# Kernel tuning notes

Hardware: AMD Instinct MI355X
Metric: run time of the kernel (lower is better)

## Reference

```python
import jax, jax.numpy as jnp
import numpy as np

L, H, LATENT, DM, DH, FF = 4, 4, 256, 768, 192, 1024
EPS = 1e-6      # fast_transformers RecurrentLinearAttention eps
LN_EPS = 1e-5


def make_pe(d_model=LATENT, max_len=5000):
    pos = np.arange(max_len, dtype=np.float32)[:, None]
    div = np.exp(np.arange(0, d_model, 2, dtype=np.float32) * (-np.log(10000.0) / d_model))
    pe = np.zeros((max_len, d_model), np.float32)
    pe[:, 0::2] = np.sin(pos * div)
    pe[:, 1::2] = np.cos(pos * div)
    return jnp.asarray(pe)

PE = make_pe()


def layer_norm(x, g, b):
    m = x.mean(-1, keepdims=True)
    v = ((x - m) ** 2).mean(-1, keepdims=True)
    return (x - m) * jax.lax.rsqrt(v + LN_EPS) * g + b


def setup_inputs() -> dict:
    key = jax.random.key(0)
    ks = jax.random.split(key, 16)
    bs, nj, nf, T, A, C = 8, 25, 6, 80, 6, 12
    s = 0.02
    return dict(
        x=jax.random.normal(ks[0], (bs, nj, nf, T), jnp.float32),
        y=jax.random.randint(ks[1], (bs, A), 0, C),
        ind_map=jnp.sort(jax.random.randint(ks[2], (T, bs), 0, A), axis=0),
        act_tstamps=jnp.sort(jax.random.randint(ks[3], (bs, A), 1, T + 1), axis=1).at[:, -1].set(T),
        skel_W=jax.random.normal(ks[4], (nj * nf, LATENT), jnp.float32) * s,
        skel_b=jnp.zeros((LATENT,), jnp.float32),
        muQuery=jax.random.normal(ks[5], (C, LATENT), jnp.float32),
        sigmaQuery=jax.random.normal(ks[6], (C, LATENT), jnp.float32),
        Wq=jax.random.normal(ks[7], (L, DM, DM), jnp.float32) * s,
        bq=jnp.zeros((L, DM), jnp.float32),
        Wk=jax.random.normal(ks[8], (L, DM, DM), jnp.float32) * s,
        bk=jnp.zeros((L, DM), jnp.float32),
        Wv=jax.random.normal(ks[9], (L, DM, DM), jnp.float32) * s,
        bv=jnp.zeros((L, DM), jnp.float32),
        Wo=jax.random.normal(ks[10], (L, DM, DM), jnp.float32) * s,
        bo=jnp.zeros((L, DM), jnp.float32),
        W1=jax.random.normal(ks[11], (L, DM, FF), jnp.float32) * s,
        b1=jnp.zeros((L, FF), jnp.float32),
        W2=jax.random.normal(ks[12], (L, FF, DM), jnp.float32) * s,
        b2=jnp.zeros((L, DM), jnp.float32),
        ln1_g=jnp.ones((L, DM), jnp.float32), ln1_b=jnp.zeros((L, DM), jnp.float32),
        ln2_g=jnp.ones((L, DM), jnp.float32), ln2_b=jnp.zeros((L, DM), jnp.float32),
        lnf_g=jnp.ones((DM,), jnp.float32), lnf_b=jnp.zeros((DM,), jnp.float32),
    )


def _fwd(x, y, ind_map, act_tstamps, skel_W, skel_b, muQuery, sigmaQuery,
         Wq, bq, Wk, bk, Wv, bv, Wo, bo, W1, b1, W2, b2,
         ln1_g, ln1_b, ln2_g, ln2_b, lnf_g, lnf_b):
    bs, nj, nf, T = x.shape
    # skeleton embedding: [T, bs, njoints*nfeats] @ W -> [T, bs, LATENT]
    xe = x.transpose(3, 0, 1, 2).reshape(T, bs, nj * nf) @ skel_W + skel_b
    mu_q = muQuery[y]        # [bs, A, LATENT]
    sig_q = sigmaQuery[y]
    barange = jnp.arange(bs)

    @jax.checkpoint
    def step(carry, inputs):
        S, Z = carry                         # [L,bs,H,DH,DH], [L,bs,H,DH]
        t, xt, ind_t = inputs
        cm = mu_q[barange, ind_t]            # gather per-sample current action query
        cs = sig_q[barange, ind_t]
        xseq = jnp.stack([cm, cs, xt], 0)    # [3, bs, LATENT]
        start = jnp.where(t == 0, 0, t + 2)  # PositionalEncoding(last_pos=t, offset=2)
        pe3 = jax.lax.dynamic_slice_in_dim(PE, start, 3, 0)
        xseq = xseq + pe3[:, None, :]
        h = xseq.transpose(1, 0, 2).reshape(bs, 3 * LATENT)  # flatten -> [bs, DM]
        nS, nZ = [], []
        for l in range(L):
            q = (h @ Wq[l] + bq[l]).reshape(bs, H, DH)
            k = (h @ Wk[l] + bk[l]).reshape(bs, H, DH)
            v = (h @ Wv[l] + bv[l]).reshape(bs, H, DH)
            Q = jax.nn.elu(q) + 1.0          # linear-attention feature map
            K = jax.nn.elu(k) + 1.0
            Sl = S[l] + K[..., :, None] * v[..., None, :]   # state update S += k (x) v
            Zl = Z[l] + K
            inv = 1.0 / (jnp.einsum('bhd,bhd->bh', Q, Zl) + EPS)
            att = jnp.einsum('bhd,bhdm,bh->bhm', Q, Sl, inv).reshape(bs, DM)
            h1 = layer_norm(h + att @ Wo[l] + bo[l], ln1_g[l], ln1_b[l])
            ffn = jax.nn.relu(h1 @ W1[l] + b1[l]) @ W2[l] + b2[l]
            h = layer_norm(h1 + ffn, ln2_g[l], ln2_b[l])
            nS.append(Sl); nZ.append(Zl)
        h = layer_norm(h, lnf_g, lnf_b)      # encoder final norm
        return (jnp.stack(nS), jnp.stack(nZ)), h

    S0 = jnp.zeros((L, bs, H, DH, DH), x.dtype)
    Z0 = jnp.zeros((L, bs, H, DH), x.dtype)
    _, finals = jax.lax.scan(step, (S0, Z0), (jnp.arange(T), xe, ind_map))  # finals: [T,bs,DM]
    tsel = jnp.maximum(act_tstamps - 1, 0)                       # [bs, A]
    mu = finals[:, :, :LATENT][tsel, barange[:, None]]           # [bs, A, LATENT]
    logvar = finals[:, :, LATENT:2 * LATENT][tsel, barange[:, None]]
    return mu, logvar


def reference(x, y, ind_map, act_tstamps, skel_W, skel_b, muQuery, sigmaQuery,
              Wq, bq, Wk, bk, Wv, bv, Wo, bo, W1, b1, W2, b2,
              ln1_g, ln1_b, ln2_g, ln2_b, lnf_g, lnf_b):
    return _fwd(x, y, ind_map, act_tstamps, skel_W, skel_b, muQuery, sigmaQuery,
                Wq, bq, Wk, bk, Wv, bv, Wo, bo, W1, b1, W2, b2,
                ln1_g, ln1_b, ln2_g, ln2_b, lnf_g, lnf_b)
```

## Files before the change

### kernel.cpp

```cpp
#include <hip/hip_runtime.h>
#include <math.h>

#define TT 80
#define BS 8
#define NA 6
#define DMODEL 768
#define NH 4
#define DH 192
#define FFD 1024
#define NROWS (TT*BS)
#define NQKV (3*DMODEL)

typedef __bf16 bf16;
typedef __bf16 bf16x8 __attribute__((ext_vector_type(8)));
typedef float  f32x4  __attribute__((ext_vector_type(4)));

__device__ __forceinline__ float block_reduce_sum256(float v, float* sm4) {
#pragma unroll
    for (int off = 32; off > 0; off >>= 1) v += __shfl_down(v, off, 64);
    int lane = threadIdx.x & 63, wid = threadIdx.x >> 6;
    if (lane == 0) sm4[wid] = v;
    __syncthreads();
    float r = sm4[0] + sm4[1] + sm4[2] + sm4[3];
    __syncthreads();
    return r;
}

__global__ __launch_bounds__(256) void embed_k(
        const float* __restrict__ x, const int* __restrict__ y,
        const int* __restrict__ ind_map, const float* __restrict__ skel_W,
        const float* __restrict__ skel_b, const float* __restrict__ muQ,
        const float* __restrict__ sigQ, float* __restrict__ h0,
        bf16* __restrict__ h0b) {
    __shared__ float xrow[152];
    int r = blockIdx.x;
    int t = r >> 3, b = r & 7;
    int c = threadIdx.x;
    if (c < 150) xrow[c] = x[(b * 150 + c) * TT + t];
    __syncthreads();
    float acc = skel_b[c];
    for (int jf = 0; jf < 150; jf++) acc += xrow[jf] * skel_W[jf * 256 + c];
    int ind_t = ind_map[t * 8 + b];
    int yb = y[b * NA + ind_t];
    float cm = muQ[yb * 256 + c];
    float cs = sigQ[yb * 256 + c];
    int start = (t == 0) ? 0 : (t + 2);
    float div = expf((float)(c & ~1) * (-9.210340371976184f / 256.0f));
    float p0, p1, p2;
    if (c & 1) {
        p0 = cosf((float)start * div);
        p1 = cosf((float)(start + 1) * div);
        p2 = cosf((float)(start + 2) * div);
    } else {
        p0 = sinf((float)start * div);
        p1 = sinf((float)(start + 1) * div);
        p2 = sinf((float)(start + 2) * div);
    }
    float* hr = h0 + (size_t)r * DMODEL;
    float v0 = cm + p0, v1 = cs + p1, v2 = acc + p2;
    hr[c] = v0; hr[c + 256] = v1; hr[c + 512] = v2;
    bf16* hb = h0b + (size_t)r * DMODEL;
    hb[c] = (bf16)v0; hb[c + 256] = (bf16)v1; hb[c + 512] = (bf16)v2;
}

__global__ __launch_bounds__(256) void transpose_k(
        const float* __restrict__ Wq, const float* __restrict__ Wk,
        const float* __restrict__ Wv, const float* __restrict__ Wo,
        const float* __restrict__ W1, const float* __restrict__ W2,
        bf16* __restrict__ qkvT, bf16* __restrict__ woT,
        bf16* __restrict__ w1T, bf16* __restrict__ w2T) {
    int lz = blockIdx.z;
    int l = lz >> 2, z = lz & 3;
    int K = (z == 3) ? 1024 : 768;
    int N = (z == 0) ? 2304 : (z == 2) ? 1024 : 768;
    int k0 = blockIdx.x * 32, n0 = blockIdx.y * 32;
    if (k0 >= K || n0 >= N) return;
    const float* src; bf16* dst; int ldsrc; int ncol;
    if (z == 0) {
        if (n0 < 768)       { src = Wq + (size_t)l * 768 * 768; ncol = n0; }
        else if (n0 < 1536) { src = Wk + (size_t)l * 768 * 768; ncol = n0 - 768; }
        else                { src = Wv + (size_t)l * 768 * 768; ncol = n0 - 1536; }
        dst = qkvT + (size_t)l * NQKV * DMODEL; ldsrc = 768;
    } else if (z == 1) { src = Wo + (size_t)l * 768 * 768;  dst = woT + (size_t)l * 768 * 768;  ldsrc = 768;  ncol = n0; }
    else if (z == 2)   { src = W1 + (size_t)l * 768 * 1024; dst = w1T + (size_t)l * 1024 * 768; ldsrc = 1024; ncol = n0; }
    else               { src = W2 + (size_t)l * 1024 * 768; dst = w2T + (size_t)l * 768 * 1024; ldsrc = 768;  ncol = n0; }
    __shared__ float tile[32][33];
    int tx = threadIdx.x & 31, ty = threadIdx.x >> 5;
#pragma unroll
    for (int i = 0; i < 4; i++) {
        int r = ty + 8 * i;
        tile[r][tx] = src[(size_t)(k0 + r) * ldsrc + ncol + tx];
    }
    __syncthreads();
#pragma unroll
    for (int i = 0; i < 4; i++) {
        int r = ty + 8 * i;
        dst[(size_t)(n0 + r) * K + k0 + tx] = (bf16)tile[tx][r];
    }
}

template <int EPI>
__global__ __launch_bounds__(256) void gemm_mfma(
        const bf16* __restrict__ A, const bf16* __restrict__ Bt,
        const float* __restrict__ bias_q, const float* __restrict__ bias_k,
        const float* __restrict__ bias_v, const float* __restrict__ resid,
        float* __restrict__ outF, bf16* __restrict__ outB,
        int M, int N, int K) {
    __shared__ __attribute__((aligned(16))) bf16 As0[64][40];
    __shared__ __attribute__((aligned(16))) bf16 As1[64][40];
    __shared__ __attribute__((aligned(16))) bf16 Bs0[64][40];
    __shared__ __attribute__((aligned(16))) bf16 Bs1[64][40];
    int tid = threadIdx.x;
    int m0 = blockIdx.y * 64, n0 = blockIdx.x * 64;
    int w = tid >> 6;
    int l = tid & 63;
    int lm = l & 15, lq = l >> 4;
    int sr = tid >> 2;
    int sk = (tid & 3) * 8;
    const bf16* Arow = &A[(size_t)(m0 + sr) * K];
    const bf16* Brow = &Bt[(size_t)(n0 + sr) * K];
    f32x4 acc[4] = {};
    uint4 a0 = *(const uint4*)&Arow[sk];
    uint4 a1 = *(const uint4*)&Arow[32 + sk];
    uint4 b0 = *(const uint4*)&Brow[sk];
    uint4 b1 = *(const uint4*)&Brow[32 + sk];
    for (int k0 = 0; k0 < K; k0 += 64) {
        __syncthreads();
        *(uint4*)&As0[sr][sk] = a0;
        *(uint4*)&As1[sr][sk] = a1;
        *(uint4*)&Bs0[sr][sk] = b0;
        *(uint4*)&Bs1[sr][sk] = b1;
        __syncthreads();
        int k2 = k0 + 64; if (k2 >= K) k2 = 0;
        a0 = *(const uint4*)&Arow[k2 + sk];
        a1 = *(const uint4*)&Arow[k2 + 32 + sk];
        b0 = *(const uint4*)&Brow[k2 + sk];
        b1 = *(const uint4*)&Brow[k2 + 32 + sk];
        bf16x8 af0 = *(bf16x8*)&As0[w * 16 + lm][lq * 8];
        bf16x8 af1 = *(bf16x8*)&As1[w * 16 + lm][lq * 8];
#pragma unroll
        for (int nb = 0; nb < 4; nb++) {
            bf16x8 bf0 = *(bf16x8*)&Bs0[nb * 16 + lm][lq * 8];
            acc[nb] = __builtin_amdgcn_mfma_f32_16x16x32_bf16(af0, bf0, acc[nb], 0, 0, 0);
        }
#pragma unroll
        for (int nb = 0; nb < 4; nb++) {
            bf16x8 bf1 = *(bf16x8*)&Bs1[nb * 16 + lm][lq * 8];
            acc[nb] = __builtin_amdgcn_mfma_f32_16x16x32_bf16(af1, bf1, acc[nb], 0, 0, 0);
        }
    }
#pragma unroll
    for (int nb = 0; nb < 4; nb++) {
        int col = n0 + nb * 16 + lm;
        float b;
        bool do_elu = false;
        if (EPI == 0) {
            if (col < 768)       { b = bias_q[col];        do_elu = true; }
            else if (col < 1536) { b = bias_k[col - 768];  do_elu = true; }
            else                 { b = bias_v[col - 1536]; }
        } else {
            b = bias_q[col];
        }
#pragma unroll
        for (int r = 0; r < 4; r++) {
            int row = m0 + w * 16 + lq * 4 + r;
            float v = acc[nb][r] + b;
            if (EPI == 0) {
                if (do_elu) v = (v > 0.0f) ? (v + 1.0f) : expf(v);
                outB[(size_t)row * N + col] = (bf16)v;
            } else if (EPI == 1) {
                v += resid[(size_t)row * N + col];
                outF[(size_t)row * N + col] = v;
            } else {
                v = fmaxf(v, 0.0f);
                outB[(size_t)row * N + col] = (bf16)v;
            }
        }
    }
}

__global__ __launch_bounds__(256) void ln_k(
        const float* __restrict__ in, float* __restrict__ outF,
        bf16* __restrict__ outB,
        const float* __restrict__ g, const float* __restrict__ b) {
    int wave = threadIdx.x >> 6, lane = threadIdx.x & 63;
    int row = blockIdx.x * 4 + wave;
    const float* xr = in + (size_t)row * DMODEL;
    float4 v[3];
    float s = 0.0f;
#pragma unroll
    for (int j = 0; j < 3; j++) {
        v[j] = *(const float4*)&xr[lane * 4 + 256 * j];
        s += v[j].x + v[j].y + v[j].z + v[j].w;
    }
#pragma unroll
    for (int mk = 1; mk < 64; mk <<= 1) s += __shfl_xor(s, mk, 64);
    float m = s * (1.0f / 768.0f);
    float sq = 0.0f;
#pragma unroll
    for (int j = 0; j < 3; j++) {
        v[j].x -= m; v[j].y -= m; v[j].z -= m; v[j].w -= m;
        sq += v[j].x * v[j].x + v[j].y * v[j].y + v[j].z * v[j].z + v[j].w * v[j].w;
    }
#pragma unroll
    for (int mk = 1; mk < 64; mk <<= 1) sq += __shfl_xor(sq, mk, 64);
    float r = rsqrtf(sq * (1.0f / 768.0f) + 1e-5f);
    float* orow = outF + (size_t)row * DMODEL;
    bf16* brow = outB + (size_t)row * DMODEL;
#pragma unroll
    for (int j = 0; j < 3; j++) {
        int c = lane * 4 + 256 * j;
        float4 gg = *(const float4*)&g[c];
        float4 bb = *(const float4*)&b[c];
        float o0 = v[j].x * r * gg.x + bb.x;
        float o1 = v[j].y * r * gg.y + bb.y;
        float o2 = v[j].z * r * gg.z + bb.z;
        float o3 = v[j].w * r * gg.w + bb.w;
        *(float4*)&orow[c] = make_float4(o0, o1, o2, o3);
        bf16 tmp4[4] = {(bf16)o0, (bf16)o1, (bf16)o2, (bf16)o3};
        *(uint2*)&brow[c] = *(uint2*)tmp4;
    }
}

__global__ __launch_bounds__(320) void attn_k(
        const bf16* __restrict__ qkvB, bf16* __restrict__ att) {
    __shared__ __attribute__((aligned(16))) char smem[64000];
    bf16* Qs = (bf16*)smem;
    bf16* Ks = (bf16*)(smem + 32000);
    bf16* Aij = (bf16*)smem;
    bf16* VT = (bf16*)(smem + 16640);

    int b = blockIdx.x >> 2, h = blockIdx.x & 3;
    int tid = threadIdx.x;
    int w = tid >> 6, l = tid & 63;
    int lm = l & 15, lq = l >> 4;

    uint4 vreg[6];
#pragma unroll
    for (int u = 0; u < 6; u++) {
        int c = tid + 320 * u;
        int t = c / 24, cc = c % 24;
        int d0 = cc * 8;
        size_t g = (size_t)(t * 8 + b) * NQKV + h * DH + d0;
        uint4 qv = *(const uint4*)&qkvB[g];
        uint4 kv = *(const uint4*)&qkvB[g + 768];
        vreg[u]  = *(const uint4*)&qkvB[g + 1536];
        *(uint4*)&Qs[t * 200 + d0] = qv;
        *(uint4*)&Ks[t * 200 + d0] = kv;
    }
    __syncthreads();

    f32x4 acc[5] = {};
#pragma unroll
    for (int k0 = 0; k0 < 192; k0 += 32) {
        bf16x8 af = *(bf16x8*)&Qs[(w * 16 + lm) * 200 + lq * 8 + k0];
#pragma unroll
        for (int nb = 0; nb < 5; nb++) {
            bf16x8 bfr = *(bf16x8*)&Ks[(nb * 16 + lm) * 200 + lq * 8 + k0];
            acc[nb] = __builtin_amdgcn_mfma_f32_16x16x32_bf16(af, bfr, acc[nb], 0, 0, 0);
        }
    }
    float mval[5][4];
    float rs[4] = {0.f, 0.f, 0.f, 0.f};
#pragma unroll
    for (int nb = 0; nb < 5; nb++)
#pragma unroll
        for (int r = 0; r < 4; r++) {
            int t = w * 16 + lq * 4 + r, tau = nb * 16 + lm;
            float v = (tau <= t) ? acc[nb][r] : 0.0f;
            mval[nb][r] = v;
            rs[r] += v;
        }
#pragma unroll
    for (int mk = 1; mk < 16; mk <<= 1)
#pragma unroll
        for (int r = 0; r < 4; r++) rs[r] += __shfl_xor(rs[r], mk, 64);
    float inv[4];
#pragma unroll
    for (int r = 0; r < 4; r++) inv[r] = 1.0f / (rs[r] + 1e-6f);

    __syncthreads();

#pragma unroll
    for (int nb = 0; nb < 5; nb++)
#pragma unroll
        for (int r = 0; r < 4; r++)
            Aij[(w * 16 + lq * 4 + r) * 104 + nb * 16 + lm] = (bf16)mval[nb][r];
    *(uint2*)&Aij[(tid >> 2) * 104 + 80 + (tid & 3) * 4] = make_uint2(0u, 0u);
#pragma unroll
    for (int u = 0; u < 6; u++) {
        int c = tid + 320 * u;
        int t = c / 24, cc = c % 24;
        int d0 = cc * 8;
        bf16 tmp8[8];
        *(uint4*)tmp8 = vreg[u];
#pragma unroll
        for (int j = 0; j < 8; j++) VT[(d0 + j) * 104 + t] = tmp8[j];
    }
    if (tid < 192) {
        *(uint4*)&VT[tid * 104 + 80] = make_uint4(0u, 0u, 0u, 0u);
        *(uint4*)&VT[tid * 104 + 88] = make_uint4(0u, 0u, 0u, 0u);
    }
    __syncthreads();

#pragma unroll 1
    for (int nc = 0; nc < 12; nc++) {
        f32x4 a2 = {};
#pragma unroll
        for (int k0 = 0; k0 < 96; k0 += 32) {
            bf16x8 af = *(bf16x8*)&Aij[(w * 16 + lm) * 104 + lq * 8 + k0];
            bf16x8 bfr = *(bf16x8*)&VT[(nc * 16 + lm) * 104 + lq * 8 + k0];
            a2 = __builtin_amdgcn_mfma_f32_16x16x32_bf16(af, bfr, a2, 0, 0, 0);
        }
#pragma unroll
        for (int r = 0; r < 4; r++) {
            int t = w * 16 + lq * 4 + r;
            att[(size_t)(t * 8 + b) * DMODEL + h * DH + nc * 16 + lm] =
                (bf16)(a2[r] * inv[r]);
        }
    }
}

__global__ __launch_bounds__(256) void final_k(
        const float* __restrict__ h, const int* __restrict__ act_ts,
        const float* __restrict__ g, const float* __restrict__ bb,
        float* __restrict__ out) {
    __shared__ float sm4[4];
    int ba = blockIdx.x;
    int b = ba / NA;
    int ts = act_ts[ba];
    int t = ts - 1; if (t < 0) t = 0;
    const float* xr = h + (size_t)(t * 8 + b) * DMODEL;
    int c = threadIdx.x;
    float x0 = xr[c], x1 = xr[c + 256], x2 = xr[c + 512];
    float m = block_reduce_sum256(x0 + x1 + x2, sm4) * (1.0f / 768.0f);
    float d0 = x0 - m, d1 = x1 - m, d2 = x2 - m;
    float v = block_reduce_sum256(d0 * d0 + d1 * d1 + d2 * d2, sm4) * (1.0f / 768.0f);
    float r = rsqrtf(v + 1e-5f);
    out[ba * 256 + c]            = d0 * r * g[c] + bb[c];
    out[48 * 256 + ba * 256 + c] = d1 * r * g[c + 256] + bb[c + 256];
}

extern "C" void kernel_launch(void* const* d_in, const int* in_sizes, int n_in,
                              void* d_out, int out_size, void* d_ws, size_t ws_size,
                              hipStream_t stream) {
    const float* x       = (const float*)d_in[0];
    const int*   y       = (const int*)d_in[1];
    const int*   ind_map = (const int*)d_in[2];
    const int*   act_ts  = (const int*)d_in[3];
    const float* skel_W  = (const float*)d_in[4];
    const float* skel_b  = (const float*)d_in[5];
    const float* muQ     = (const float*)d_in[6];
    const float* sigQ    = (const float*)d_in[7];
    const float* Wq = (const float*)d_in[8];   const float* bq = (const float*)d_in[9];
    const float* Wk = (const float*)d_in[10];  const float* bk = (const float*)d_in[11];
    const float* Wv = (const float*)d_in[12];  const float* bv = (const float*)d_in[13];
    const float* Wo = (const float*)d_in[14];  const float* bo = (const float*)d_in[15];
    const float* W1 = (const float*)d_in[16];  const float* b1 = (const float*)d_in[17];
    const float* W2 = (const float*)d_in[18];  const float* b2 = (const float*)d_in[19];
    const float* ln1_g = (const float*)d_in[20]; const float* ln1_b = (const float*)d_in[21];
    const float* ln2_g = (const float*)d_in[22]; const float* ln2_b = (const float*)d_in[23];
    const float* lnf_g = (const float*)d_in[24]; const float* lnf_b = (const float*)d_in[25];
    float* out = (float*)d_out;

    char* p = (char*)d_ws;
    const size_t R  = (size_t)NROWS * DMODEL;
    float* h    = (float*)p; p += R * 4;
    float* h1   = (float*)p; p += R * 4;
    float* tmp  = (float*)p; p += R * 4;
    bf16* qkvB  = (bf16*)p;  p += (size_t)NROWS * NQKV * 2;
    bf16* hB    = (bf16*)p;  p += R * 2;
    bf16* h1B   = (bf16*)p;  p += R * 2;
    bf16* attB  = (bf16*)p;  p += R * 2;
    bf16* ffn1B = (bf16*)p;  p += (size_t)NROWS * FFD * 2;
    bf16* qkvT  = (bf16*)p;  p += (size_t)4 * NQKV * DMODEL * 2;
    bf16* woT   = (bf16*)p;  p += (size_t)4 * DMODEL * DMODEL * 2;
    bf16* w1T   = (bf16*)p;  p += (size_t)4 * FFD * DMODEL * 2;
    bf16* w2T   = (bf16*)p;  p += (size_t)4 * DMODEL * FFD * 2;

    dim3 gT(32, 72, 16);
    transpose_k<<<gT, 256, 0, stream>>>(Wq, Wk, Wv, Wo, W1, W2, qkvT, woT, w1T, w2T);
    embed_k<<<NROWS, 256, 0, stream>>>(x, y, ind_map, skel_W, skel_b, muQ, sigQ, h, hB);

    dim3 gQKV(NQKV / 64, 10);
    dim3 g768(12, 10);
    dim3 g1024(16, 10);
    for (int l = 0; l < 4; l++) {
        const bf16* qkvTl = qkvT + (size_t)l * NQKV * DMODEL;
        const bf16* woTl  = woT  + (size_t)l * DMODEL * DMODEL;
        const bf16* w1Tl  = w1T  + (size_t)l * FFD * DMODEL;
        const bf16* w2Tl  = w2T  + (size_t)l * DMODEL * FFD;
        gemm_mfma<0><<<gQKV, 256, 0, stream>>>(hB, qkvTl,
                bq + l * DMODEL, bk + l * DMODEL, bv + l * DMODEL,
                nullptr, nullptr, qkvB, NROWS, NQKV, DMODEL);
        attn_k<<<32, 320, 0, stream>>>(qkvB, attB);
        gemm_mfma<1><<<g768, 256, 0, stream>>>(attB, woTl,
                bo + l * DMODEL, nullptr, nullptr, h, tmp, nullptr,
                NROWS, DMODEL, DMODEL);
        ln_k<<<NROWS / 4, 256, 0, stream>>>(tmp, h1, h1B, ln1_g + l * DMODEL, ln1_b + l * DMODEL);
        gemm_mfma<2><<<g1024, 256, 0, stream>>>(h1B, w1Tl,
                b1 + l * FFD, nullptr, nullptr, nullptr, nullptr, ffn1B,
                NROWS, FFD, DMODEL);
        gemm_mfma<1><<<g768, 256, 0, stream>>>(ffn1B, w2Tl,
                b2 + l * DMODEL, nullptr, nullptr, h1, tmp, nullptr,
                NROWS, DMODEL, FFD);
        ln_k<<<NROWS / 4, 256, 0, stream>>>(tmp, h, hB, ln2_g + l * DMODEL, ln2_b + l * DMODEL);
    }

    final_k<<<48, 256, 0, stream>>>(h, act_ts, lnf_g, lnf_b, out);
}
```

Baseline: 422.5 us.

## Fuse LayerNorm into GEMM epilogue stats and next GEMM's A-load prologue

Removes the standalone LayerNorm kernels. The residual GEMMs now accumulate per-row sum and sum-of-squares through atomics in their epilogue. The following GEMM then normalizes its fp32 A operand on the fly while staging it into shared memory, and one column-block writes out the normalized fp32 rows for later residual use. This saves two launches per layer and one full read/write pass of the activations. In exchange the A loads are fp32, twice the bytes, every column block repeats the normalization, the stats need a memset, and the one-pass E[x^2]-mean^2 variance is less numerically robust.

Result: slower. 464.6 us (+10.0%).

```diff
diff --git a/kernel.cpp b/kernel.cpp
--- a/kernel.cpp
+++ b/kernel.cpp
@@ -99,12 +99,16 @@
     }
 }
 
-template <int EPI>
+template <int AMODE, int EPI>
 __global__ __launch_bounds__(256) void gemm_mfma(
-        const bf16* __restrict__ A, const bf16* __restrict__ Bt,
-        const float* __restrict__ bias_q, const float* __restrict__ bias_k,
-        const float* __restrict__ bias_v, const float* __restrict__ resid,
+        const void* __restrict__ Asrc, const bf16* __restrict__ Bt,
+        const float* __restrict__ bias0, const float* __restrict__ bias1,
+        const float* __restrict__ bias2, const float* __restrict__ resid,
+        const float* __restrict__ inS, const float* __restrict__ inQ,
+        const float* __restrict__ ag, const float* __restrict__ ab,
+        float* __restrict__ aNormOut,
         float* __restrict__ outF, bf16* __restrict__ outB,
+        float* __restrict__ outS, float* __restrict__ outQ,
         int M, int N, int K) {
     __shared__ __attribute__((aligned(16))) bf16 As0[64][40];
     __shared__ __attribute__((aligned(16))) bf16 As1[64][40];
@@ -117,23 +121,77 @@
     int lm = l & 15, lq = l >> 4;
     int sr = tid >> 2;
     int sk = (tid & 3) * 8;
-    const bf16* Arow = &A[(size_t)(m0 + sr) * K];
+    const bf16* Ab = nullptr; const float* Af = nullptr;
+    float mn = 0.0f, rs = 0.0f;
+    if (AMODE == 0) {
+        Ab = (const bf16*)Asrc + (size_t)(m0 + sr) * K;
+    } else {
+        Af = (const float*)Asrc + (size_t)(m0 + sr) * 768;
+        float s = inS[m0 + sr], q = inQ[m0 + sr];
+        mn = s * (1.0f / 768.0f);
+        rs = rsqrtf(q * (1.0f / 768.0f) - mn * mn + 1e-5f);
+    }
     const bf16* Brow = &Bt[(size_t)(n0 + sr) * K];
+    bool awrite = (AMODE == 1) && (blockIdx.x == 0);
     f32x4 acc[4] = {};
-    uint4 a0 = *(const uint4*)&Arow[sk];
-    uint4 a1 = *(const uint4*)&Arow[32 + sk];
-    uint4 b0 = *(const uint4*)&Brow[sk];
-    uint4 b1 = *(const uint4*)&Brow[32 + sk];
+    uint4 a0, a1, a2, a3, b0, b1;
+    if (AMODE == 0) {
+        a0 = *(const uint4*)&Ab[sk];
+        a1 = *(const uint4*)&Ab[32 + sk];
+    } else {
+        a0 = *(const uint4*)&Af[sk];      a1 = *(const uint4*)&Af[sk + 4];
+        a2 = *(const uint4*)&Af[32 + sk]; a3 = *(const uint4*)&Af[32 + sk + 4];
+    }
+    b0 = *(const uint4*)&Brow[sk];
+    b1 = *(const uint4*)&Brow[32 + sk];
     for (int k0 = 0; k0 < K; k0 += 64) {
         __syncthreads();
-        *(uint4*)&As0[sr][sk] = a0;
-        *(uint4*)&As1[sr][sk] = a1;
+        if (AMODE == 0) {
+            *(uint4*)&As0[sr][sk] = a0;
+            *(uint4*)&As1[sr][sk] = a1;
+        } else {
+#pragma unroll
+            for (int half = 0; half < 2; half++) {
+                int kabs = k0 + 32 * half;
+                float4 v0 = *(float4*)(half ? &a2 : &a0);
+                float4 v1 = *(float4*)(half ? &a3 : &a1);
+                float4 gg0 = *(const float4*)&ag[kabs + sk];
+                float4 gg1 = *(const float4*)&ag[kabs + sk + 4];
+                float4 bb0 = *(const float4*)&ab[kabs + sk];
+                float4 bb1 = *(const float4*)&ab[kabs + sk + 4];
+                float o[8];
+                o[0] = (v0.x - mn) * rs * gg0.x + bb0.x;
+                o[1] = (v0.y - mn) * rs * gg0.y + bb0.y;
+                o[2] = (v0.z - mn) * rs * gg0.z + bb0.z;
+                o[3] = (v0.w - mn) * rs * gg0.w + bb0.w;
+                o[4] = (v1.x - mn) * rs * gg1.x + bb1.x;
+                o[5] = (v1.y - mn) * rs * gg1.y + bb1.y;
+                o[6] = (v1.z - mn) * rs * gg1.z + bb1.z;
+                o[7] = (v1.w - mn) * rs * gg1.w + bb1.w;
+                if (awrite) {
+                    *(float4*)&aNormOut[(size_t)(m0 + sr) * 768 + kabs + sk] =
+                        make_float4(o[0], o[1], o[2], o[3]);
+                    *(float4*)&aNormOut[(size_t)(m0 + sr) * 768 + kabs + sk + 4] =
+                        make_float4(o[4], o[5], o[6], o[7]);
+                }
+                bf16 t8[8];
+#pragma unroll
+                for (int j = 0; j < 8; j++) t8[j] = (bf16)o[j];
+                if (half) *(uint4*)&As1[sr][sk] = *(uint4*)t8;
+                else      *(uint4*)&As0[sr][sk] = *(uint4*)t8;
+            }
+        }
         *(uint4*)&Bs0[sr][sk] = b0;
         *(uint4*)&Bs1[sr][sk] = b1;
         __syncthreads();
         int k2 = k0 + 64; if (k2 >= K) k2 = 0;
-        a0 = *(const uint4*)&Arow[k2 + sk];
-        a1 = *(const uint4*)&Arow[k2 + 32 + sk];
+        if (AMODE == 0) {
+            a0 = *(const uint4*)&Ab[k2 + sk];
+            a1 = *(const uint4*)&Ab[k2 + 32 + sk];
+        } else {
+            a0 = *(const uint4*)&Af[k2 + sk];      a1 = *(const uint4*)&Af[k2 + sk + 4];
+            a2 = *(const uint4*)&Af[k2 + 32 + sk]; a3 = *(const uint4*)&Af[k2 + 32 + sk + 4];
+        }
         b0 = *(const uint4*)&Brow[k2 + sk];
         b1 = *(const uint4*)&Brow[k2 + 32 + sk];
         bf16x8 af0 = *(bf16x8*)&As0[w * 16 + lm][lq * 8];
@@ -149,76 +207,60 @@
             acc[nb] = __builtin_amdgcn_mfma_f32_16x16x32_bf16(af1, bf1, acc[nb], 0, 0, 0);
         }
     }
-#pragma unroll
-    for (int nb = 0; nb < 4; nb++) {
-        int col = n0 + nb * 16 + lm;
-        float b;
-        bool do_elu = false;
-        if (EPI == 0) {
-            if (col < 768)       { b = bias_q[col];        do_elu = true; }
-            else if (col < 1536) { b = bias_k[col - 768];  do_elu = true; }
-            else                 { b = bias_v[col - 1536]; }
-        } else {
-            b = bias_q[col];
-        }
-#pragma unroll
-        for (int r = 0; r < 4; r++) {
-            int row = m0 + w * 16 + lq * 4 + r;
-            float v = acc[nb][r] + b;
+    if (EPI == 3) {
+        float s[4] = {0.f, 0.f, 0.f, 0.f}, q[4] = {0.f, 0.f, 0.f, 0.f};
+#pragma unroll
+        for (int nb = 0; nb < 4; nb++) {
+            int col = n0 + nb * 16 + lm;
+            float bia = bias0[col];
+#pragma unroll
+            for (int r = 0; r < 4; r++) {
+                int row = m0 + w * 16 + lq * 4 + r;
+                float v = acc[nb][r] + bia + resid[(size_t)row * N + col];
+                outF[(size_t)row * N + col] = v;
+                s[r] += v; q[r] += v * v;
+            }
+        }
+#pragma unroll
+        for (int mk = 1; mk < 16; mk <<= 1)
+#pragma unroll
+            for (int r = 0; r < 4; r++) {
+                s[r] += __shfl_xor(s[r], mk, 64);
+                q[r] += __shfl_xor(q[r], mk, 64);
+            }
+        if (lm == 0) {
+#pragma unroll
+            for (int r = 0; r < 4; r++) {
+                int row = m0 + w * 16 + lq * 4 + r;
+                atomicAdd(&outS[row], s[r]);
+                atomicAdd(&outQ[row], q[r]);
+            }
+        }
+    } else {
+#pragma unroll
+        for (int nb = 0; nb < 4; nb++) {
+            int col = n0 + nb * 16 + lm;
+            float bia;
+            bool do_elu = false;
             if (EPI == 0) {
-                if (do_elu) v = (v > 0.0f) ? (v + 1.0f) : expf(v);
+                if (col < 768)       { bia = bias0[col];        do_elu = true; }
+                else if (col < 1536) { bia = bias1[col - 768];  do_elu = true; }
+                else                 { bia = bias2[col - 1536]; }
+            } else {
+                bia = bias0[col];
+            }
+#pragma unroll
+            for (int r = 0; r < 4; r++) {
+                int row = m0 + w * 16 + lq * 4 + r;
+                float v = acc[nb][r] + bia;
+                if (EPI == 0) {
+                    if (do_elu) v = (v > 0.0f) ? (v + 1.0f) : expf(v);
+                } else {
+                    v = fmaxf(v, 0.0f);
+                }
                 outB[(size_t)row * N + col] = (bf16)v;
-            } else if (EPI == 1) {
-                v += resid[(size_t)row * N + col];
-                outF[(size_t)row * N + col] = v;
-            } else {
-                v = fmaxf(v, 0.0f);
-                outB[(size_t)row * N + col] = (bf16)v;
-            }
-        }
-    }
-}
-
-__global__ __launch_bounds__(256) void ln_k(
-        const float* __restrict__ in, float* __restrict__ outF,
-        bf16* __restrict__ outB,
-        const float* __restrict__ g, const float* __restrict__ b) {
-    int wave = threadIdx.x >> 6, lane = threadIdx.x & 63;
-    int row = blockIdx.x * 4 + wave;
-    const float* xr = in + (size_t)row * DMODEL;
-    float4 v[3];
-    float s = 0.0f;
-#pragma unroll
-    for (int j = 0; j < 3; j++) {
-        v[j] = *(const float4*)&xr[lane * 4 + 256 * j];
-        s += v[j].x + v[j].y + v[j].z + v[j].w;
-    }
-#pragma unroll
-    for (int mk = 1; mk < 64; mk <<= 1) s += __shfl_xor(s, mk, 64);
-    float m = s * (1.0f / 768.0f);
-    float sq = 0.0f;
-#pragma unroll
-    for (int j = 0; j < 3; j++) {
-        v[j].x -= m; v[j].y -= m; v[j].z -= m; v[j].w -= m;
-        sq += v[j].x * v[j].x + v[j].y * v[j].y + v[j].z * v[j].z + v[j].w * v[j].w;
-    }
-#pragma unroll
-    for (int mk = 1; mk < 64; mk <<= 1) sq += __shfl_xor(sq, mk, 64);
-    float r = rsqrtf(sq * (1.0f / 768.0f) + 1e-5f);
-    float* orow = outF + (size_t)row * DMODEL;
-    bf16* brow = outB + (size_t)row * DMODEL;
-#pragma unroll
-    for (int j = 0; j < 3; j++) {
-        int c = lane * 4 + 256 * j;
-        float4 gg = *(const float4*)&g[c];
-        float4 bb = *(const float4*)&b[c];
-        float o0 = v[j].x * r * gg.x + bb.x;
-        float o1 = v[j].y * r * gg.y + bb.y;
-        float o2 = v[j].z * r * gg.z + bb.z;
-        float o3 = v[j].w * r * gg.w + bb.w;
-        *(float4*)&orow[c] = make_float4(o0, o1, o2, o3);
-        bf16 tmp4[4] = {(bf16)o0, (bf16)o1, (bf16)o2, (bf16)o3};
-        *(uint2*)&brow[c] = *(uint2*)tmp4;
+            }
+        }
     }
 }
 
@@ -322,23 +364,30 @@
 }
 
 __global__ __launch_bounds__(256) void final_k(
-        const float* __restrict__ h, const int* __restrict__ act_ts,
-        const float* __restrict__ g, const float* __restrict__ bb,
+        const float* __restrict__ tmp2, const float* __restrict__ sS,
+        const float* __restrict__ sQ, const int* __restrict__ act_ts,
+        const float* __restrict__ g2, const float* __restrict__ b2,
+        const float* __restrict__ gf, const float* __restrict__ bf,
         float* __restrict__ out) {
     __shared__ float sm4[4];
     int ba = blockIdx.x;
     int b = ba / NA;
     int ts = act_ts[ba];
     int t = ts - 1; if (t < 0) t = 0;
-    const float* xr = h + (size_t)(t * 8 + b) * DMODEL;
+    int row = t * 8 + b;
+    const float* xr = tmp2 + (size_t)row * DMODEL;
+    float mn = sS[row] * (1.0f / 768.0f);
+    float r2 = rsqrtf(sQ[row] * (1.0f / 768.0f) - mn * mn + 1e-5f);
     int c = threadIdx.x;
-    float x0 = xr[c], x1 = xr[c + 256], x2 = xr[c + 512];
+    float x0 = (xr[c]       - mn) * r2 * g2[c]       + b2[c];
+    float x1 = (xr[c + 256] - mn) * r2 * g2[c + 256] + b2[c + 256];
+    float x2 = (xr[c + 512] - mn) * r2 * g2[c + 512] + b2[c + 512];
     float m = block_reduce_sum256(x0 + x1 + x2, sm4) * (1.0f / 768.0f);
     float d0 = x0 - m, d1 = x1 - m, d2 = x2 - m;
     float v = block_reduce_sum256(d0 * d0 + d1 * d1 + d2 * d2, sm4) * (1.0f / 768.0f);
     float r = rsqrtf(v + 1e-5f);
-    out[ba * 256 + c]            = d0 * r * g[c] + bb[c];
-    out[48 * 256 + ba * 256 + c] = d1 * r * g[c + 256] + bb[c + 256];
+    out[ba * 256 + c]            = d0 * r * gf[c] + bf[c];
+    out[48 * 256 + ba * 256 + c] = d1 * r * gf[c + 256] + bf[c + 256];
 }
 
 extern "C" void kernel_launch(void* const* d_in, const int* in_sizes, int n_in,
@@ -365,12 +414,13 @@
 
     char* p = (char*)d_ws;
     const size_t R  = (size_t)NROWS * DMODEL;
-    float* h    = (float*)p; p += R * 4;
-    float* h1   = (float*)p; p += R * 4;
-    float* tmp  = (float*)p; p += R * 4;
+    float* hF   = (float*)p; p += R * 4;
+    float* h1F  = (float*)p; p += R * 4;
+    float* tmp1 = (float*)p; p += R * 4;
+    float* tmp2 = (float*)p; p += R * 4;
+    float* stats = (float*)p; p += 8 * 1280 * 4;
     bf16* qkvB  = (bf16*)p;  p += (size_t)NROWS * NQKV * 2;
     bf16* hB    = (bf16*)p;  p += R * 2;
-    bf16* h1B   = (bf16*)p;  p += R * 2;
     bf16* attB  = (bf16*)p;  p += R * 2;
     bf16* ffn1B = (bf16*)p;  p += (size_t)NROWS * FFD * 2;
     bf16* qkvT  = (bf16*)p;  p += (size_t)4 * NQKV * DMODEL * 2;
@@ -378,9 +428,10 @@
     bf16* w1T   = (bf16*)p;  p += (size_t)4 * FFD * DMODEL * 2;
     bf16* w2T   = (bf16*)p;  p += (size_t)4 * DMODEL * FFD * 2;
 
+    hipMemsetAsync(stats, 0, 8 * 1280 * 4, stream);
     dim3 gT(32, 72, 16);
     transpose_k<<<gT, 256, 0, stream>>>(Wq, Wk, Wv, Wo, W1, W2, qkvT, woT, w1T, w2T);
-    embed_k<<<NROWS, 256, 0, stream>>>(x, y, ind_map, skel_W, skel_b, muQ, sigQ, h, hB);
+    embed_k<<<NROWS, 256, 0, stream>>>(x, y, ind_map, skel_W, skel_b, muQ, sigQ, hF, hB);
 
     dim3 gQKV(NQKV / 64, 10);
     dim3 g768(12, 10);
@@ -390,22 +441,36 @@
         const bf16* woTl  = woT  + (size_t)l * DMODEL * DMODEL;
         const bf16* w1Tl  = w1T  + (size_t)l * FFD * DMODEL;
         const bf16* w2Tl  = w2T  + (size_t)l * DMODEL * FFD;
-        gemm_mfma<0><<<gQKV, 256, 0, stream>>>(hB, qkvTl,
-                bq + l * DMODEL, bk + l * DMODEL, bv + l * DMODEL,
-                nullptr, nullptr, qkvB, NROWS, NQKV, DMODEL);
+        float* sS1 = stats + (size_t)(l * 2 + 0) * 1280; float* sQ1 = sS1 + 640;
+        float* sS2 = stats + (size_t)(l * 2 + 1) * 1280; float* sQ2 = sS2 + 640;
+        if (l == 0) {
+            gemm_mfma<0, 0><<<gQKV, 256, 0, stream>>>(hB, qkvTl,
+                    bq, bk, bv, nullptr,
+                    nullptr, nullptr, nullptr, nullptr, nullptr,
+                    nullptr, qkvB, nullptr, nullptr, NROWS, NQKV, DMODEL);
+        } else {
+            float* pS2 = stats + (size_t)((l - 1) * 2 + 1) * 1280; float* pQ2 = pS2 + 640;
+            gemm_mfma<1, 0><<<gQKV, 256, 0, stream>>>(tmp2, qkvTl,
+                    bq + l * DMODEL, bk + l * DMODEL, bv + l * DMODEL, nullptr,
+                    pS2, pQ2, ln2_g + (l - 1) * DMODEL, ln2_b + (l - 1) * DMODEL, hF,
+                    nullptr, qkvB, nullptr, nullptr, NROWS, NQKV, DMODEL);
+        }
         attn_k<<<32, 320, 0, stream>>>(qkvB, attB);
-        gemm_mfma<1><<<g768, 256, 0, stream>>>(attB, woTl,
-                bo + l * DMODEL, nullptr, nullptr, h, tmp, nullptr,
-                NROWS, DMODEL, DMODEL);
-        ln_k<<<NROWS / 4, 256, 0, stream>>>(tmp, h1, h1B, ln1_g + l * DMODEL, ln1_b + l * DMODEL);
-        gemm_mfma<2><<<g1024, 256, 0, stream>>>(h1B, w1Tl,
-                b1 + l * FFD, nullptr, nullptr, nullptr, nullptr, ffn1B,
-                NROWS, FFD, DMODEL);
-        gemm_mfma<1><<<g768, 256, 0, stream>>>(ffn1B, w2Tl,
-                b2 + l * DMODEL, nullptr, nullptr, h1, tmp, nullptr,
-                NROWS, DMODEL, FFD);
-        ln_k<<<NROWS / 4, 256, 0, stream>>>(tmp, h, hB, ln2_g + l * DMODEL, ln2_b + l * DMODEL);
-    }
-
-    final_k<<<48, 256, 0, stream>>>(h, act_ts, lnf_g, lnf_b, out);
-}
+        gemm_mfma<0, 3><<<g768, 256, 0, stream>>>(attB, woTl,
+                bo + l * DMODEL, nullptr, nullptr, hF,
+                nullptr, nullptr, nullptr, nullptr, nullptr,
+                tmp1, nullptr, sS1, sQ1, NROWS, DMODEL, DMODEL);
+        gemm_mfma<1, 2><<<g1024, 256, 0, stream>>>(tmp1, w1Tl,
+                b1 + l * FFD, nullptr, nullptr, nullptr,
+                sS1, sQ1, ln1_g + l * DMODEL, ln1_b + l * DMODEL, h1F,
+                nullptr, ffn1B, nullptr, nullptr, NROWS, FFD, DMODEL);
+        gemm_mfma<0, 3><<<g768, 256, 0, stream>>>(ffn1B, w2Tl,
+                b2 + l * DMODEL, nullptr, nullptr, h1F,
+                nullptr, nullptr, nullptr, nullptr, nullptr,
+                tmp2, nullptr, sS2, sQ2, NROWS, DMODEL, FFD);
+    }
+
+    float* sS2_3 = stats + (size_t)(3 * 2 + 1) * 1280; float* sQ2_3 = sS2_3 + 640;
+    final_k<<<48, 256, 0, stream>>>(tmp2, sS2_3, sQ2_3, act_ts,
+            ln2_g + 3 * DMODEL, ln2_b + 3 * DMODEL, lnf_g, lnf_b, out);
+}
```

## Load GEMM MFMA fragments directly from global memory, dropping LDS staging

Applied to the files above, without the earlier changes.

The MFMA GEMM no longer stages A and B tiles through shared memory with barriers. Each wave now loads its bf16x8 fragments straight from global memory with a compile-time K and an unrolled loop. This removes the LDS writes, the LDS reads and the __syncthreads per K step for these small GEMMs. The cost is that the four waves of a block each fetch the same B fragments and each lane reads a strided pattern, which leans on L1/L2 caching and may lower effective bandwidth.

Measured after the change: 561.1 us. 32.8% more time.

```diff
diff --git a/kernel.cpp b/kernel.cpp
--- a/kernel.cpp
+++ b/kernel.cpp
@@ -99,54 +99,28 @@
     }
 }
 
-template <int EPI>
-__global__ __launch_bounds__(256) void gemm_mfma(
+template <int K, int EPI>
+__global__ __launch_bounds__(256) void gemm_direct(
         const bf16* __restrict__ A, const bf16* __restrict__ Bt,
         const float* __restrict__ bias_q, const float* __restrict__ bias_k,
         const float* __restrict__ bias_v, const float* __restrict__ resid,
         float* __restrict__ outF, bf16* __restrict__ outB,
-        int M, int N, int K) {
-    __shared__ __attribute__((aligned(16))) bf16 As0[64][40];
-    __shared__ __attribute__((aligned(16))) bf16 As1[64][40];
-    __shared__ __attribute__((aligned(16))) bf16 Bs0[64][40];
-    __shared__ __attribute__((aligned(16))) bf16 Bs1[64][40];
+        int M, int N) {
     int tid = threadIdx.x;
     int m0 = blockIdx.y * 64, n0 = blockIdx.x * 64;
     int w = tid >> 6;
     int l = tid & 63;
     int lm = l & 15, lq = l >> 4;
-    int sr = tid >> 2;
-    int sk = (tid & 3) * 8;
-    const bf16* Arow = &A[(size_t)(m0 + sr) * K];
-    const bf16* Brow = &Bt[(size_t)(n0 + sr) * K];
+    const bf16* Arow = A + (size_t)(m0 + w * 16 + lm) * K + lq * 8;
+    const bf16* Brow = Bt + (size_t)(n0 + lm) * K + lq * 8;
     f32x4 acc[4] = {};
-    uint4 a0 = *(const uint4*)&Arow[sk];
-    uint4 a1 = *(const uint4*)&Arow[32 + sk];
-    uint4 b0 = *(const uint4*)&Brow[sk];
-    uint4 b1 = *(const uint4*)&Brow[32 + sk];
-    for (int k0 = 0; k0 < K; k0 += 64) {
-        __syncthreads();
-        *(uint4*)&As0[sr][sk] = a0;
-        *(uint4*)&As1[sr][sk] = a1;
-        *(uint4*)&Bs0[sr][sk] = b0;
-        *(uint4*)&Bs1[sr][sk] = b1;
-        __syncthreads();
-        int k2 = k0 + 64; if (k2 >= K) k2 = 0;
-        a0 = *(const uint4*)&Arow[k2 + sk];
-        a1 = *(const uint4*)&Arow[k2 + 32 + sk];
-        b0 = *(const uint4*)&Brow[k2 + sk];
-        b1 = *(const uint4*)&Brow[k2 + 32 + sk];
-        bf16x8 af0 = *(bf16x8*)&As0[w * 16 + lm][lq * 8];
-        bf16x8 af1 = *(bf16x8*)&As1[w * 16 + lm][lq * 8];
+#pragma unroll 8
+    for (int k0 = 0; k0 < K; k0 += 32) {
+        bf16x8 af = *(const bf16x8*)&Arow[k0];
 #pragma unroll
         for (int nb = 0; nb < 4; nb++) {
-            bf16x8 bf0 = *(bf16x8*)&Bs0[nb * 16 + lm][lq * 8];
-            acc[nb] = __builtin_amdgcn_mfma_f32_16x16x32_bf16(af0, bf0, acc[nb], 0, 0, 0);
-        }
-#pragma unroll
-        for (int nb = 0; nb < 4; nb++) {
-            bf16x8 bf1 = *(bf16x8*)&Bs1[nb * 16 + lm][lq * 8];
-            acc[nb] = __builtin_amdgcn_mfma_f32_16x16x32_bf16(af1, bf1, acc[nb], 0, 0, 0);
+            bf16x8 bfr = *(const bf16x8*)&Brow[(size_t)nb * 16 * K + k0];
+            acc[nb] = __builtin_amdgcn_mfma_f32_16x16x32_bf16(af, bfr, acc[nb], 0, 0, 0);
         }
     }
 #pragma unroll
@@ -390,20 +364,20 @@
         const bf16* woTl  = woT  + (size_t)l * DMODEL * DMODEL;
         const bf16* w1Tl  = w1T  + (size_t)l * FFD * DMODEL;
         const bf16* w2Tl  = w2T  + (size_t)l * DMODEL * FFD;
-        gemm_mfma<0><<<gQKV, 256, 0, stream>>>(hB, qkvTl,
+        gemm_direct<768, 0><<<gQKV, 256, 0, stream>>>(hB, qkvTl,
                 bq + l * DMODEL, bk + l * DMODEL, bv + l * DMODEL,
-                nullptr, nullptr, qkvB, NROWS, NQKV, DMODEL);
+                nullptr, nullptr, qkvB, NROWS, NQKV);
         attn_k<<<32, 320, 0, stream>>>(qkvB, attB);
-        gemm_mfma<1><<<g768, 256, 0, stream>>>(attB, woTl,
+        gemm_direct<768, 1><<<g768, 256, 0, stream>>>(attB, woTl,
                 bo + l * DMODEL, nullptr, nullptr, h, tmp, nullptr,
-                NROWS, DMODEL, DMODEL);
+                NROWS, DMODEL);
         ln_k<<<NROWS / 4, 256, 0, stream>>>(tmp, h1, h1B, ln1_g + l * DMODEL, ln1_b + l * DMODEL);
-        gemm_mfma<2><<<g1024, 256, 0, stream>>>(h1B, w1Tl,
+        gemm_direct<768, 2><<<g1024, 256, 0, stream>>>(h1B, w1Tl,
                 b1 + l * FFD, nullptr, nullptr, nullptr, nullptr, ffn1B,
-                NROWS, FFD, DMODEL);
-        gemm_mfma<1><<<g768, 256, 0, stream>>>(ffn1B, w2Tl,
+                NROWS, FFD);
+        gemm_direct<1024, 1><<<g768, 256, 0, stream>>>(ffn1B, w2Tl,
                 b2 + l * DMODEL, nullptr, nullptr, h1, tmp, nullptr,
-                NROWS, DMODEL, FFD);
+                NROWS, DMODEL);
         ln_k<<<NROWS / 4, 256, 0, stream>>>(tmp, h, hB, ln2_g + l * DMODEL, ln2_b + l * DMODEL);
     }
 
```
